# Optimization experiments

Hardware: AMD Instinct MI355X
Metric: run time of the kernel (lower is better)

## Reference

```python
import jax, jax.numpy as jnp
import numpy as np

DT = 10.0 / 200  # 0.05
DX = 20.0 / 128  # 0.15625

# 5x5 fixed finite-difference stencils (torch Conv2d = cross-correlation, so use as-is)
_LAPL = np.array([[0, 0, -1/12, 0, 0],
                  [0, 0,  4/3,  0, 0],
                  [-1/12, 4/3, -5, 4/3, -1/12],
                  [0, 0,  4/3,  0, 0],
                  [0, 0, -1/12, 0, 0]], dtype=np.float32)
_PAR_X = np.array([[0, 0,  1/12, 0, 0],
                   [0, 0, -8/12, 0, 0],
                   [0, 0,  0,    0, 0],
                   [0, 0,  8/12, 0, 0],
                   [0, 0, -1/12, 0, 0]], dtype=np.float32)


def _conv2d_valid(x, kern):
    # x: [N, 1, H, W], kern: [5, 5] -> [N, 1, H-4, W-4]
    return jax.lax.conv_general_dilated(x, jnp.asarray(kern)[None, None], (1, 1), 'VALID')


def _time_deriv(x):
    # x: [T, B, 1, h, w]; central diff interior, one-sided at endpoints (all /DT)
    interior = (x[2:] - x[:-2]) / (2.0 * DT)
    t0 = (-1.5 * x[0] + 2.0 * x[1] - 0.5 * x[2]) / DT
    tn = (0.5 * x[-3] - 2.0 * x[-2] + 1.5 * x[-1]) / DT
    return jnp.concatenate([t0[None], interior, tn[None]], axis=0)


def setup_inputs() -> dict:
    key = jax.random.key(0)
    output = jax.random.normal(key, (20, 8, 3, 256, 256), dtype=jnp.float32)
    return {"output": output}


def reference(output):
    T, B, C, H, W = output.shape
    u = output[:, :, 1:2]  # [T,B,1,H,W]
    v = output[:, :, 2:3]

    lap_u = _conv2d_valid(u.reshape(T * B, 1, H, W), _LAPL).reshape(T, B, 1, H - 4, W - 4) / (DX ** 2)
    lap_v = _conv2d_valid(v.reshape(T * B, 1, H, W), _LAPL).reshape(T, B, 1, H - 4, W - 4) / (DX ** 2)

    uc = u[:, :, :, 2:-2, 2:-2]  # [T,B,1,H-4,W-4]
    vc = v[:, :, :, 2:-2, 2:-2]
    u_t = _time_deriv(uc)
    v_t = _time_deriv(vc)

    Du, Dv = 0.16, 0.08
    f, k = 0.06, 0.062
    f_u = Du * lap_u - uc * vc ** 2 + f * (1.0 - uc) - u_t
    f_v = Dv * lap_v + uc * vc ** 2 - (f + k) * vc - v_t
    return (f_u, f_v)
```

## Files before the change

kernel.cpp:

```cpp
#include <hip/hip_runtime.h>


#define IN_W   256
#define IN_H   256
#define OUT_W  252
#define OUT_H  252
#define T_DIM  20
#define B_DIM  8

__global__ __launch_bounds__(256) void gs_loss_kernel(
    const float* __restrict__ in, float* __restrict__ out, int total)
{
    int idx = blockIdx.x * blockDim.x + threadIdx.x;
    if (idx >= total) return;

    int x    = idx % OUT_W;
    int rest = idx / OUT_W;
    int y    = rest % OUT_H;
    int tb   = rest / OUT_H;
    int b    = tb & 7;
    int t    = tb >> 3;

    const int planeStride = IN_H * IN_W;
    const int bStride     = 3 * planeStride;
    const int tStride     = B_DIM * bStride;

    const float* __restrict__ up = in + (long)t * tStride + (long)b * bStride + planeStride;
    const float* __restrict__ vp = up + planeStride;

    int off = (y + 2) * IN_W + (x + 2);

    float uc = up[off];
    float vc = vp[off];

    const float c1 = 4.0f / 3.0f;
    const float c2 = 1.0f / 12.0f;

    float lap_u = c1 * (up[off - 1] + up[off + 1] + up[off - IN_W] + up[off + IN_W])
                - c2 * (up[off - 2] + up[off + 2] + up[off - 2 * IN_W] + up[off + 2 * IN_W])
                - 5.0f * uc;
    float lap_v = c1 * (vp[off - 1] + vp[off + 1] + vp[off - IN_W] + vp[off + IN_W])
                - c2 * (vp[off - 2] + vp[off + 2] + vp[off - 2 * IN_W] + vp[off + 2 * IN_W])
                - 5.0f * vc;

    const float inv_dx2 = 1.0f / (0.15625f * 0.15625f);
    lap_u *= inv_dx2;
    lap_v *= inv_dx2;

    const float inv_dt = 20.0f;
    float u_t, v_t;
    if (t == 0) {
        float u1 = up[off + tStride], u2 = up[off + 2 * tStride];
        float v1 = vp[off + tStride], v2 = vp[off + 2 * tStride];
        u_t = (-1.5f * uc + 2.0f * u1 - 0.5f * u2) * inv_dt;
        v_t = (-1.5f * vc + 2.0f * v1 - 0.5f * v2) * inv_dt;
    } else if (t == T_DIM - 1) {
        float um1 = up[off - tStride], um2 = up[off - 2 * tStride];
        float vm1 = vp[off - tStride], vm2 = vp[off - 2 * tStride];
        u_t = (0.5f * um2 - 2.0f * um1 + 1.5f * uc) * inv_dt;
        v_t = (0.5f * vm2 - 2.0f * vm1 + 1.5f * vc) * inv_dt;
    } else {
        u_t = (up[off + tStride] - up[off - tStride]) * (0.5f * inv_dt);
        v_t = (vp[off + tStride] - vp[off - tStride]) * (0.5f * inv_dt);
    }

    const float Du = 0.16f, Dv = 0.08f, fRate = 0.06f, kRate = 0.062f;
    float uvv = uc * vc * vc;
    float f_u = Du * lap_u - uvv + fRate * (1.0f - uc) - u_t;
    float f_v = Dv * lap_v + uvv - (fRate + kRate) * vc - v_t;

    out[idx]         = f_u;
    out[idx + total] = f_v;
}

extern "C" void kernel_launch(void* const* d_in, const int* in_sizes, int n_in,
                              void* d_out, int out_size, void* d_ws, size_t ws_size,
                              hipStream_t stream) {
    const float* in = (const float*)d_in[0];
    float* out = (float*)d_out;

    const int total = T_DIM * B_DIM * OUT_H * OUT_W;
    const int threads = 256;
    const int blocks = (total + threads - 1) / threads;
    gs_loss_kernel<<<blocks, threads, 0, stream>>>(in, out, total);
}
```

Baseline: 224.1 us.

## March each thread over time with register sliding window and float2 vectorized loads

Each thread now owns two adjacent output columns at one (b,y) and loops over all T, keeping the previous centre values and Laplacians in registers. This removes the repeated global reads of neighbouring time steps for the time derivative and removes per-thread index division. Loads and stores become float2. The grid shrinks to 2016*128 threads, each doing serial work over 20 steps, which lowers parallelism and the number of loads in flight per thread.

```diff
diff --git a/kernel.cpp b/kernel.cpp
--- a/kernel.cpp
+++ b/kernel.cpp
@@ -2,75 +2,133 @@
 
 
 #define IN_W   256
-#define IN_H   256
 #define OUT_W  252
 #define OUT_H  252
 #define T_DIM  20
 #define B_DIM  8
 
 __global__ __launch_bounds__(256) void gs_loss_kernel(
-    const float* __restrict__ in, float* __restrict__ out, int total)
+    const float* __restrict__ in, float* __restrict__ out)
 {
-    int idx = blockIdx.x * blockDim.x + threadIdx.x;
-    if (idx >= total) return;
+    int gid = blockIdx.x * blockDim.x + threadIdx.x;
+    int xg  = gid & 127;
+    if (xg >= 126) return;
+    int r   = gid >> 7;
+    int b   = r & 7;
+    int y   = r >> 3;
+    int x0  = xg * 2;
 
-    int x    = idx % OUT_W;
-    int rest = idx / OUT_W;
-    int y    = rest % OUT_H;
-    int tb   = rest / OUT_H;
-    int b    = tb & 7;
-    int t    = tb >> 3;
-
-    const int planeStride = IN_H * IN_W;
+    const int planeStride = IN_W * IN_W;
     const int bStride     = 3 * planeStride;
     const int tStride     = B_DIM * bStride;
 
-    const float* __restrict__ up = in + (long)t * tStride + (long)b * bStride + planeStride;
-    const float* __restrict__ vp = up + planeStride;
+    const float* base = in + (size_t)b * bStride + planeStride
+                           + (size_t)(y + 2) * IN_W + (x0 + 2);
 
-    int off = (y + 2) * IN_W + (x + 2);
+    const int tOut = B_DIM * OUT_H * OUT_W;
+    const int total = T_DIM * tOut;
+    float* outu = out + ((size_t)b * OUT_H + y) * OUT_W + x0;
+    float* outv = outu + total;
 
-    float uc = up[off];
-    float vc = vp[off];
+    const float c1      = 4.0f / 3.0f;
+    const float c2      = 1.0f / 12.0f;
+    const float inv_dx2 = 1.0f / (0.15625f * 0.15625f);
+    const float inv_dt  = 20.0f;
+    const float Du = 0.16f, Dv = 0.08f, fR = 0.06f, kR = 0.062f;
 
-    const float c1 = 4.0f / 3.0f;
-    const float c2 = 1.0f / 12.0f;
+    float2 u_cm2 = {0,0}, u_cm1 = {0,0}, u_cc = {0,0}, u_lm1 = {0,0}, u_l0 = {0,0};
+    float2 v_cm2 = {0,0}, v_cm1 = {0,0}, v_cc = {0,0}, v_lm1 = {0,0}, v_l0 = {0,0};
 
-    float lap_u = c1 * (up[off - 1] + up[off + 1] + up[off - IN_W] + up[off + IN_W])
-                - c2 * (up[off - 2] + up[off + 2] + up[off - 2 * IN_W] + up[off + 2 * IN_W])
-                - 5.0f * uc;
-    float lap_v = c1 * (vp[off - 1] + vp[off + 1] + vp[off - IN_W] + vp[off + IN_W])
-                - c2 * (vp[off - 2] + vp[off + 2] + vp[off - 2 * IN_W] + vp[off + 2 * IN_W])
-                - 5.0f * vc;
+    for (int t = 0; t < T_DIM; ++t) {
+        const float* up = base + (size_t)t * tStride;
+        const float* vp = up + planeStride;
 
-    const float inv_dx2 = 1.0f / (0.15625f * 0.15625f);
-    lap_u *= inv_dx2;
-    lap_v *= inv_dx2;
+        float2 u_ym2 = *(const float2*)(up - 2 * IN_W);
+        float2 u_ym1 = *(const float2*)(up - IN_W);
+        float2 u_a   = *(const float2*)(up - 2);
+        float2 u_c   = *(const float2*)(up);
+        float2 u_e   = *(const float2*)(up + 2);
+        float2 u_yp1 = *(const float2*)(up + IN_W);
+        float2 u_yp2 = *(const float2*)(up + 2 * IN_W);
 
-    const float inv_dt = 20.0f;
-    float u_t, v_t;
-    if (t == 0) {
-        float u1 = up[off + tStride], u2 = up[off + 2 * tStride];
-        float v1 = vp[off + tStride], v2 = vp[off + 2 * tStride];
-        u_t = (-1.5f * uc + 2.0f * u1 - 0.5f * u2) * inv_dt;
-        v_t = (-1.5f * vc + 2.0f * v1 - 0.5f * v2) * inv_dt;
-    } else if (t == T_DIM - 1) {
-        float um1 = up[off - tStride], um2 = up[off - 2 * tStride];
-        float vm1 = vp[off - tStride], vm2 = vp[off - 2 * tStride];
-        u_t = (0.5f * um2 - 2.0f * um1 + 1.5f * uc) * inv_dt;
-        v_t = (0.5f * vm2 - 2.0f * vm1 + 1.5f * vc) * inv_dt;
-    } else {
-        u_t = (up[off + tStride] - up[off - tStride]) * (0.5f * inv_dt);
-        v_t = (vp[off + tStride] - vp[off - tStride]) * (0.5f * inv_dt);
+        float2 v_ym2 = *(const float2*)(vp - 2 * IN_W);
+        float2 v_ym1 = *(const float2*)(vp - IN_W);
+        float2 v_a   = *(const float2*)(vp - 2);
+        float2 v_c   = *(const float2*)(vp);
+        float2 v_e   = *(const float2*)(vp + 2);
+        float2 v_yp1 = *(const float2*)(vp + IN_W);
+        float2 v_yp2 = *(const float2*)(vp + 2 * IN_W);
+
+        float2 lu, lv;
+        lu.x = (c1 * (u_a.y + u_c.y + u_ym1.x + u_yp1.x)
+              - c2 * (u_a.x + u_e.x + u_ym2.x + u_yp2.x)
+              - 5.0f * u_c.x) * inv_dx2;
+        lu.y = (c1 * (u_c.x + u_e.x + u_ym1.y + u_yp1.y)
+              - c2 * (u_a.y + u_e.y + u_ym2.y + u_yp2.y)
+              - 5.0f * u_c.y) * inv_dx2;
+        lv.x = (c1 * (v_a.y + v_c.y + v_ym1.x + v_yp1.x)
+              - c2 * (v_a.x + v_e.x + v_ym2.x + v_yp2.x)
+              - 5.0f * v_c.x) * inv_dx2;
+        lv.y = (c1 * (v_c.x + v_e.x + v_ym1.y + v_yp1.y)
+              - c2 * (v_a.y + v_e.y + v_ym2.y + v_yp2.y)
+              - 5.0f * v_c.y) * inv_dx2;
+
+        float2 ucn = u_c;
+        float2 vcn = v_c;
+
+        if (t == 0) { u_l0 = lu; v_l0 = lv; }
+
+        if (t == 2) {
+            float2 ut, vt, fu, fv;
+            ut.x = (-1.5f * u_cm1.x + 2.0f * u_cc.x - 0.5f * ucn.x) * inv_dt;
+            ut.y = (-1.5f * u_cm1.y + 2.0f * u_cc.y - 0.5f * ucn.y) * inv_dt;
+            vt.x = (-1.5f * v_cm1.x + 2.0f * v_cc.x - 0.5f * vcn.x) * inv_dt;
+            vt.y = (-1.5f * v_cm1.y + 2.0f * v_cc.y - 0.5f * vcn.y) * inv_dt;
+            float uvvx = u_cm1.x * v_cm1.x * v_cm1.x;
+            float uvvy = u_cm1.y * v_cm1.y * v_cm1.y;
+            fu.x = Du * u_l0.x - uvvx + fR * (1.0f - u_cm1.x) - ut.x;
+            fu.y = Du * u_l0.y - uvvy + fR * (1.0f - u_cm1.y) - ut.y;
+            fv.x = Dv * v_l0.x + uvvx - (fR + kR) * v_cm1.x - vt.x;
+            fv.y = Dv * v_l0.y + uvvy - (fR + kR) * v_cm1.y - vt.y;
+            *(float2*)(outu) = fu;
+            *(float2*)(outv) = fv;
+        }
+
+        if (t >= 2) {
+            float2 ut, vt, fu, fv;
+            ut.x = (ucn.x - u_cm1.x) * (0.5f * inv_dt);
+            ut.y = (ucn.y - u_cm1.y) * (0.5f * inv_dt);
+            vt.x = (vcn.x - v_cm1.x) * (0.5f * inv_dt);
+            vt.y = (vcn.y - v_cm1.y) * (0.5f * inv_dt);
+            float uvvx = u_cc.x * v_cc.x * v_cc.x;
+            float uvvy = u_cc.y * v_cc.y * v_cc.y;
+            fu.x = Du * u_lm1.x - uvvx + fR * (1.0f - u_cc.x) - ut.x;
+            fu.y = Du * u_lm1.y - uvvy + fR * (1.0f - u_cc.y) - ut.y;
+            fv.x = Dv * v_lm1.x + uvvx - (fR + kR) * v_cc.x - vt.x;
+            fv.y = Dv * v_lm1.y + uvvy - (fR + kR) * v_cc.y - vt.y;
+            *(float2*)(outu + (size_t)(t - 1) * tOut) = fu;
+            *(float2*)(outv + (size_t)(t - 1) * tOut) = fv;
+        }
+
+        u_cm2 = u_cm1; u_cm1 = u_cc; u_cc = ucn; u_lm1 = lu;
+        v_cm2 = v_cm1; v_cm1 = v_cc; v_cc = vcn; v_lm1 = lv;
     }
 
-    const float Du = 0.16f, Dv = 0.08f, fRate = 0.06f, kRate = 0.062f;
-    float uvv = uc * vc * vc;
-    float f_u = Du * lap_u - uvv + fRate * (1.0f - uc) - u_t;
-    float f_v = Dv * lap_v + uvv - (fRate + kRate) * vc - v_t;
-
-    out[idx]         = f_u;
-    out[idx + total] = f_v;
+    {
+        float2 ut, vt, fu, fv;
+        ut.x = (0.5f * u_cm2.x - 2.0f * u_cm1.x + 1.5f * u_cc.x) * inv_dt;
+        ut.y = (0.5f * u_cm2.y - 2.0f * u_cm1.y + 1.5f * u_cc.y) * inv_dt;
+        vt.x = (0.5f * v_cm2.x - 2.0f * v_cm1.x + 1.5f * v_cc.x) * inv_dt;
+        vt.y = (0.5f * v_cm2.y - 2.0f * v_cm1.y + 1.5f * v_cc.y) * inv_dt;
+        float uvvx = u_cc.x * v_cc.x * v_cc.x;
+        float uvvy = u_cc.y * v_cc.y * v_cc.y;
+        fu.x = Du * u_lm1.x - uvvx + fR * (1.0f - u_cc.x) - ut.x;
+        fu.y = Du * u_lm1.y - uvvy + fR * (1.0f - u_cc.y) - ut.y;
+        fv.x = Dv * v_lm1.x + uvvx - (fR + kR) * v_cc.x - vt.x;
+        fv.y = Dv * v_lm1.y + uvvy - (fR + kR) * v_cc.y - vt.y;
+        *(float2*)(outu + (size_t)(T_DIM - 1) * tOut) = fu;
+        *(float2*)(outv + (size_t)(T_DIM - 1) * tOut) = fv;
+    }
 }
 
 extern "C" void kernel_launch(void* const* d_in, const int* in_sizes, int n_in,
@@ -79,8 +137,7 @@
     const float* in = (const float*)d_in[0];
     float* out = (float*)d_out;
 
-    const int total = T_DIM * B_DIM * OUT_H * OUT_W;
     const int threads = 256;
-    const int blocks = (total + threads - 1) / threads;
-    gs_loss_kernel<<<blocks, threads, 0, stream>>>(in, out, total);
+    const int blocks = (2016 * 128) / threads;
+    gs_loss_kernel<<<blocks, threads, 0, stream>>>(in, out);
 }
```

New measurement: 233.7 us. +4.3%, slower.

## Stream time dimension per thread with register reuse and float4 vectorized stencil

Applied to the files above, without the earlier changes.

Each thread now handles four adjacent x outputs and walks along time in a rolling register window. Center values and Laplacians are reused across time steps, so the extra loads for the time derivative go away. Loads are vectorized as float4/float2 and outputs are written as float4. The time axis is split into two halves per block to keep some parallelism, but the grid shrinks to 1008 blocks, with one of every 64 lanes idle. This lowers occupancy and relies on per-thread sequential loop latency.

```diff
diff --git a/kernel.cpp b/kernel.cpp
--- a/kernel.cpp
+++ b/kernel.cpp
@@ -1,76 +1,126 @@
 #include <hip/hip_runtime.h>
 
 
-#define IN_W   256
-#define IN_H   256
-#define OUT_W  252
-#define OUT_H  252
-#define T_DIM  20
-#define B_DIM  8
+#define T_OUT (8 * 252 * 252)
+
+#define GS_INT(c) { \
+    float ut = (ucn.c - u_cm1.c) * hdt; \
+    float vt = (vcn.c - v_cm1.c) * hdt; \
+    float uvv = u_cc.c * v_cc.c * v_cc.c; \
+    fu.c = Du * u_lm1.c - uvv + fR * (1.0f - u_cc.c) - ut; \
+    fv.c = Dv * v_lm1.c + uvv - (fR + kR) * v_cc.c - vt; }
+
+#define GS_T0(c) { \
+    float ut = (-1.5f * u_cm1.c + 2.0f * u_cc.c - 0.5f * ucn.c) * inv_dt; \
+    float vt = (-1.5f * v_cm1.c + 2.0f * v_cc.c - 0.5f * vcn.c) * inv_dt; \
+    float uvv = u_cm1.c * v_cm1.c * v_cm1.c; \
+    fu.c = Du * u_l0.c - uvv + fR * (1.0f - u_cm1.c) - ut; \
+    fv.c = Dv * v_l0.c + uvv - (fR + kR) * v_cm1.c - vt; }
+
+#define GS_TN(c) { \
+    float ut = (0.5f * u_cm2.c - 2.0f * u_cm1.c + 1.5f * u_cc.c) * inv_dt; \
+    float vt = (0.5f * v_cm2.c - 2.0f * v_cm1.c + 1.5f * v_cc.c) * inv_dt; \
+    float uvv = u_cc.c * v_cc.c * v_cc.c; \
+    fu.c = Du * u_lm1.c - uvv + fR * (1.0f - u_cc.c) - ut; \
+    fv.c = Dv * v_lm1.c + uvv - (fR + kR) * v_cc.c - vt; }
 
 __global__ __launch_bounds__(256) void gs_loss_kernel(
-    const float* __restrict__ in, float* __restrict__ out, int total)
+    const float* __restrict__ in, float* __restrict__ out)
 {
-    int idx = blockIdx.x * blockDim.x + threadIdx.x;
-    if (idx >= total) return;
+    const int tid  = threadIdx.x;
+    const int xg   = tid & 63;
+    const int yloc = tid >> 6;
+    if (xg >= 63) return;
 
-    int x    = idx % OUT_W;
-    int rest = idx / OUT_W;
-    int y    = rest % OUT_H;
-    int tb   = rest / OUT_H;
-    int b    = tb & 7;
-    int t    = tb >> 3;
+    const int bidx  = blockIdx.x;
+    const int b     = bidx & 7;
+    const int rest  = bidx >> 3;
+    const int ytile = rest % 63;
+    const int h     = rest / 63;
 
-    const int planeStride = IN_H * IN_W;
+    const int y  = ytile * 4 + yloc;
+    const int x0 = xg * 4;
+
+    const int planeStride = 256 * 256;
     const int bStride     = 3 * planeStride;
-    const int tStride     = B_DIM * bStride;
+    const int tStride     = 8 * bStride;
 
-    const float* __restrict__ up = in + (long)t * tStride + (long)b * bStride + planeStride;
-    const float* __restrict__ vp = up + planeStride;
+    const float* ubase = in + (size_t)b * bStride + planeStride
+                         + (size_t)(y + 2) * 256 + x0;
 
-    int off = (y + 2) * IN_W + (x + 2);
+    const int total = 20 * T_OUT;
+    float* outu = out + ((size_t)b * 252 + y) * 252 + x0;
+    float* outv = outu + total;
 
-    float uc = up[off];
-    float vc = vp[off];
+    const float C1 = 4.0f / 3.0f, C2 = 1.0f / 12.0f;
+    const float inv_dx2 = 1.0f / (0.15625f * 0.15625f);
+    const float inv_dt  = 20.0f;
+    const float hdt     = 10.0f;
+    const float Du = 0.16f, Dv = 0.08f, fR = 0.06f, kR = 0.062f;
 
-    const float c1 = 4.0f / 3.0f;
-    const float c2 = 1.0f / 12.0f;
+    float4 u_cm2{}, u_cm1{}, u_cc{}, u_lm1{}, u_l0{};
+    float4 v_cm2{}, v_cm1{}, v_cc{}, v_lm1{}, v_l0{};
 
-    float lap_u = c1 * (up[off - 1] + up[off + 1] + up[off - IN_W] + up[off + IN_W])
-                - c2 * (up[off - 2] + up[off + 2] + up[off - 2 * IN_W] + up[off + 2 * IN_W])
-                - 5.0f * uc;
-    float lap_v = c1 * (vp[off - 1] + vp[off + 1] + vp[off - IN_W] + vp[off + IN_W])
-                - c2 * (vp[off - 2] + vp[off + 2] + vp[off - 2 * IN_W] + vp[off + 2 * IN_W])
-                - 5.0f * vc;
+    const int t_begin = h ? 9 : 0;
 
-    const float inv_dx2 = 1.0f / (0.15625f * 0.15625f);
-    lap_u *= inv_dx2;
-    lap_v *= inv_dx2;
+    for (int i = 0; i <= 10; ++i) {
+        const int t = t_begin + i;
+        const float* up = ubase + (size_t)t * tStride;
+        const float* vp = up + planeStride;
 
-    const float inv_dt = 20.0f;
-    float u_t, v_t;
-    if (t == 0) {
-        float u1 = up[off + tStride], u2 = up[off + 2 * tStride];
-        float v1 = vp[off + tStride], v2 = vp[off + 2 * tStride];
-        u_t = (-1.5f * uc + 2.0f * u1 - 0.5f * u2) * inv_dt;
-        v_t = (-1.5f * vc + 2.0f * v1 - 0.5f * v2) * inv_dt;
-    } else if (t == T_DIM - 1) {
-        float um1 = up[off - tStride], um2 = up[off - 2 * tStride];
-        float vm1 = vp[off - tStride], vm2 = vp[off - 2 * tStride];
-        u_t = (0.5f * um2 - 2.0f * um1 + 1.5f * uc) * inv_dt;
-        v_t = (0.5f * vm2 - 2.0f * vm1 + 1.5f * vc) * inv_dt;
-    } else {
-        u_t = (up[off + tStride] - up[off - tStride]) * (0.5f * inv_dt);
-        v_t = (vp[off + tStride] - vp[off - tStride]) * (0.5f * inv_dt);
+        float4 uL = *(const float4*)(up);
+        float4 uR = *(const float4*)(up + 4);
+        float2 um1a = *(const float2*)(up - 256 + 2), um1b = *(const float2*)(up - 256 + 4);
+        float2 up1a = *(const float2*)(up + 256 + 2), up1b = *(const float2*)(up + 256 + 4);
+        float2 um2a = *(const float2*)(up - 512 + 2), um2b = *(const float2*)(up - 512 + 4);
+        float2 up2a = *(const float2*)(up + 512 + 2), up2b = *(const float2*)(up + 512 + 4);
+
+        float4 vL = *(const float4*)(vp);
+        float4 vR = *(const float4*)(vp + 4);
+        float2 vm1a = *(const float2*)(vp - 256 + 2), vm1b = *(const float2*)(vp - 256 + 4);
+        float2 vp1a = *(const float2*)(vp + 256 + 2), vp1b = *(const float2*)(vp + 256 + 4);
+        float2 vm2a = *(const float2*)(vp - 512 + 2), vm2b = *(const float2*)(vp - 512 + 4);
+        float2 vp2a = *(const float2*)(vp + 512 + 2), vp2b = *(const float2*)(vp + 512 + 4);
+
+        float4 lu, lv;
+        lu.x = (C1*(uL.y + uL.w + um1a.x + up1a.x) - C2*(uL.x + uR.x + um2a.x + up2a.x) - 5.0f*uL.z) * inv_dx2;
+        lu.y = (C1*(uL.z + uR.x + um1a.y + up1a.y) - C2*(uL.y + uR.y + um2a.y + up2a.y) - 5.0f*uL.w) * inv_dx2;
+        lu.z = (C1*(uL.w + uR.y + um1b.x + up1b.x) - C2*(uL.z + uR.z + um2b.x + up2b.x) - 5.0f*uR.x) * inv_dx2;
+        lu.w = (C1*(uR.x + uR.z + um1b.y + up1b.y) - C2*(uL.w + uR.w + um2b.y + up2b.y) - 5.0f*uR.y) * inv_dx2;
+        lv.x = (C1*(vL.y + vL.w + vm1a.x + vp1a.x) - C2*(vL.x + vR.x + vm2a.x + vp2a.x) - 5.0f*vL.z) * inv_dx2;
+        lv.y = (C1*(vL.z + vR.x + vm1a.y + vp1a.y) - C2*(vL.y + vR.y + vm2a.y + vp2a.y) - 5.0f*vL.w) * inv_dx2;
+        lv.z = (C1*(vL.w + vR.y + vm1b.x + vp1b.x) - C2*(vL.z + vR.z + vm2b.x + vp2b.x) - 5.0f*vR.x) * inv_dx2;
+        lv.w = (C1*(vR.x + vR.z + vm1b.y + vp1b.y) - C2*(vL.w + vR.w + vm2b.y + vp2b.y) - 5.0f*vR.y) * inv_dx2;
+
+        float4 ucn = make_float4(uL.z, uL.w, uR.x, uR.y);
+        float4 vcn = make_float4(vL.z, vL.w, vR.x, vR.y);
+
+        if (h == 0 && i == 0) { u_l0 = lu; v_l0 = lv; }
+
+        if (h == 0 && i == 2) {
+            float4 fu, fv;
+            GS_T0(x); GS_T0(y); GS_T0(z); GS_T0(w);
+            *(float4*)(outu) = fu;
+            *(float4*)(outv) = fv;
+        }
+
+        if (i >= 2) {
+            float4 fu, fv;
+            GS_INT(x); GS_INT(y); GS_INT(z); GS_INT(w);
+            *(float4*)(outu + (size_t)(t - 1) * T_OUT) = fu;
+            *(float4*)(outv + (size_t)(t - 1) * T_OUT) = fv;
+        }
+
+        u_cm2 = u_cm1; u_cm1 = u_cc; u_cc = ucn; u_lm1 = lu;
+        v_cm2 = v_cm1; v_cm1 = v_cc; v_cc = vcn; v_lm1 = lv;
     }
 
-    const float Du = 0.16f, Dv = 0.08f, fRate = 0.06f, kRate = 0.062f;
-    float uvv = uc * vc * vc;
-    float f_u = Du * lap_u - uvv + fRate * (1.0f - uc) - u_t;
-    float f_v = Dv * lap_v + uvv - (fRate + kRate) * vc - v_t;
-
-    out[idx]         = f_u;
-    out[idx + total] = f_v;
+    if (h == 1) {
+        float4 fu, fv;
+        GS_TN(x); GS_TN(y); GS_TN(z); GS_TN(w);
+        *(float4*)(outu + (size_t)19 * T_OUT) = fu;
+        *(float4*)(outv + (size_t)19 * T_OUT) = fv;
+    }
 }
 
 extern "C" void kernel_launch(void* const* d_in, const int* in_sizes, int n_in,
@@ -79,8 +129,6 @@
     const float* in = (const float*)d_in[0];
     float* out = (float*)d_out;
 
-    const int total = T_DIM * B_DIM * OUT_H * OUT_W;
-    const int threads = 256;
-    const int blocks = (total + threads - 1) / threads;
-    gs_loss_kernel<<<blocks, threads, 0, stream>>>(in, out, total);
+    const int blocks = 8 * 63 * 2;
+    gs_loss_kernel<<<blocks, 256, 0, stream>>>(in, out);
 }
```

Result: faster. 201.8 us (-9.9%).
